# Kernel tuning notes

Hardware: AMD Instinct MI355X
Metric: run time of the kernel (lower is better)

## Reference

```python
import jax, jax.numpy as jnp
import numpy as np

N_HEAD = 16
LN_EPS = 1e-5


def _layernorm(x, g, b):
    mu = jnp.mean(x, axis=-1, keepdims=True)
    var = jnp.mean(jnp.square(x - mu), axis=-1, keepdims=True)
    return (x - mu) * jax.lax.rsqrt(var + LN_EPS) * g + b


def setup_inputs() -> dict:
    key = jax.random.key(0)
    ks = jax.random.split(key, 8)
    B, T, C = 2, 2048, 1024
    Dff = 4 * C
    s = 0.02
    return {
        "x": jax.random.normal(ks[0], (B, T, C), jnp.float32),
        "wq": jax.random.normal(ks[1], (C, C), jnp.float32) * s,
        "wk": jax.random.normal(ks[2], (C, C), jnp.float32) * s,
        "wv": jax.random.normal(ks[3], (C, C), jnp.float32) * s,
        "w_proj": jax.random.normal(ks[4], (C, C), jnp.float32) * s,
        "b_proj": jnp.zeros((C,), jnp.float32),
        "w1": jax.random.normal(ks[5], (C, Dff), jnp.float32) * s,
        "b1": jnp.zeros((Dff,), jnp.float32),
        "w2": jax.random.normal(ks[6], (Dff, C), jnp.float32) * s,
        "b2": jnp.zeros((C,), jnp.float32),
        "g1": jnp.ones((C,), jnp.float32),
        "be1": jnp.zeros((C,), jnp.float32),
        "g2": jnp.ones((C,), jnp.float32),
        "be2": jnp.zeros((C,), jnp.float32),
    }


def reference(x, wq, wk, wv, w_proj, b_proj, w1, b1, w2, b2, g1, be1, g2, be2):
    B, T, C = x.shape
    H = N_HEAD
    hd = C // H
    # QKV projections (all heads folded into one matmul each), -> [B,H,T,hd]
    q = (x @ wq).reshape(B, T, H, hd).transpose(0, 2, 1, 3)
    k = (x @ wk).reshape(B, T, H, hd).transpose(0, 2, 1, 3)
    v = (x @ wv).reshape(B, T, H, hd).transpose(0, 2, 1, 3)
    # scaled causal attention; scale = head_size ** -0.5 as in torch source
    scores = jnp.einsum("bhqd,bhkd->bhqk", q, k) * (hd ** -0.5)
    causal = jnp.tril(jnp.ones((T, T), bool))
    scores = jnp.where(causal, scores, jnp.finfo(scores.dtype).min)
    wei = jax.nn.softmax(scores, axis=-1)
    attn = jnp.einsum("bhqk,bhkd->bhqd", wei, v)  # [B,H,T,hd]
    attn = attn.transpose(0, 2, 1, 3).reshape(B, T, C)
    y = attn @ w_proj + b_proj
    # post-LN residuals as in Block.forward
    x = _layernorm(x + y, g1, be1)
    y = jnp.maximum(x @ w1 + b1, 0.0) @ w2 + b2
    x = _layernorm(x + y, g2, be2)
    return x
```

## Files before the change

### kernel.cpp

```cpp
#include <hip/hip_runtime.h>
#include <hip/hip_bf16.h>


typedef __attribute__((ext_vector_type(8))) short bf16x8;
typedef __attribute__((ext_vector_type(4))) float f32x4;
typedef __attribute__((ext_vector_type(4))) short short4v;

__device__ inline short f2bf(float f) {
    __hip_bfloat16 h = __float2bfloat16(f);
    return *reinterpret_cast<short*>(&h);
}


__global__ __launch_bounds__(256) void convert_f2b(const float* __restrict__ in,
                                                   short* __restrict__ out, int n4) {
    int i = blockIdx.x * 256 + threadIdx.x;
    if (i < n4) {
        float4 v = *(const float4*)(in + (size_t)i * 4);
        short4v o = { f2bf(v.x), f2bf(v.y), f2bf(v.z), f2bf(v.w) };
        *(short4v*)(out + (size_t)i * 4) = o;
    }
}

__global__ __launch_bounds__(256) void transpose4_f2b(const float* __restrict__ s0,
                                                      const float* __restrict__ s1,
                                                      const float* __restrict__ s2,
                                                      const float* __restrict__ s3,
                                                      short* __restrict__ d0,
                                                      short* __restrict__ d1,
                                                      short* __restrict__ d2,
                                                      short* __restrict__ d3,
                                                      float scale0) {
    __shared__ short tile[32][33];
    const int z = blockIdx.z;
    const float* in = z == 0 ? s0 : z == 1 ? s1 : z == 2 ? s2 : s3;
    short* out = z == 0 ? d0 : z == 1 ? d1 : z == 2 ? d2 : d3;
    const float scale = z == 0 ? scale0 : 1.0f;
    int c0 = blockIdx.x * 32, r0 = blockIdx.y * 32;
    int tx = threadIdx.x, ty = threadIdx.y;
    for (int i = ty; i < 32; i += 8)
        tile[i][tx] = f2bf(in[(size_t)(r0 + i) * 1024 + c0 + tx] * scale);
    __syncthreads();
    for (int i = ty; i < 32; i += 8)
        out[(size_t)(c0 + i) * 1024 + r0 + tx] = tile[tx][i];
}

__global__ __launch_bounds__(256) void transpose_f2b(const float* __restrict__ in,
                                                     short* __restrict__ out, int R, int C,
                                                     float scale) {
    __shared__ short tile[32][33];
    int c0 = blockIdx.x * 32, r0 = blockIdx.y * 32;
    int tx = threadIdx.x, ty = threadIdx.y;
    for (int i = ty; i < 32; i += 8)
        tile[i][tx] = f2bf(in[(size_t)(r0 + i) * C + c0 + tx] * scale);
    __syncthreads();
    for (int i = ty; i < 32; i += 8)
        out[(size_t)(c0 + i) * R + r0 + tx] = tile[tx][i];
}

__global__ __launch_bounds__(256) void transpose_b2b(const short* __restrict__ in,
                                                     short* __restrict__ out, int R, int C,
                                                     int istride) {
    __shared__ short tile[32][33];
    int c0 = blockIdx.x * 32, r0 = blockIdx.y * 32;
    int tx = threadIdx.x, ty = threadIdx.y;
    for (int i = ty; i < 32; i += 8)
        tile[i][tx] = in[(size_t)(r0 + i) * istride + c0 + tx];
    __syncthreads();
    for (int i = ty; i < 32; i += 8)
        out[(size_t)(c0 + i) * R + r0 + tx] = tile[tx][i];
}

template <int BN, int BIAS, int RELU, int OUTBF>
__global__ __launch_bounds__(256) void gemm_bt(const short* __restrict__ A,
                                               const short* __restrict__ BT,
                                               const float* __restrict__ bias,
                                               void* __restrict__ Cout,
                                               int M, int N, int K, int lda, int ldb,
                                               void* __restrict__ Cout2) {
    constexpr int NI = BN / 32;
    __shared__ short As[128 * 32];
    __shared__ short Bs[BN * 32];
    const int tid = threadIdx.x;
    const int wid = tid >> 6;
    const int lane = tid & 63;
    const int wr = wid >> 1, wc = wid & 1;
    const int kz = blockIdx.z;
    if (kz) { A += K; BT += K; Cout = Cout2; }
    const int gx = gridDim.x;
    int flat = blockIdx.x + gx * blockIdx.y;
    const int nwg = gx * gridDim.y;
    int w = flat;
    if ((nwg & 7) == 0) {
        const int q = nwg >> 3;
        w = (flat & 7) * q + (flat >> 3);
    }
    const int row0 = (w % gx) * 128;
    const int col0 = (w / gx) * BN;
    const int lr = lane & 15;
    const int lk = (lane >> 4) * 8;
    const int sr = lane >> 2;
    const int sc = (lane & 3) * 8;

    f32x4 acc[4][NI] = {};
    for (int k = 0; k < K; k += 32) {
#pragma unroll
        for (int c = 0; c < 2; ++c) {
            const int ch = wid + c * 4;
            const short* ga = A + (size_t)(row0 + ch * 16 + sr) * lda + k + sc;
            __builtin_amdgcn_global_load_lds(
                (const __attribute__((address_space(1))) unsigned int*)ga,
                (__attribute__((address_space(3))) unsigned int*)(As + ch * 512), 16, 0, 0);
        }
#pragma unroll
        for (int c = 0; c < BN / 64; ++c) {
            const int ch = wid + c * 4;
            const short* gb = BT + (size_t)(col0 + ch * 16 + sr) * ldb + k + sc;
            __builtin_amdgcn_global_load_lds(
                (const __attribute__((address_space(1))) unsigned int*)gb,
                (__attribute__((address_space(3))) unsigned int*)(Bs + ch * 512), 16, 0, 0);
        }
        __syncthreads();
        bf16x8 a[4], b[NI];
#pragma unroll
        for (int m = 0; m < 4; ++m)
            a[m] = *(const bf16x8*)(As + (wr * 64 + m * 16 + lr) * 32 + lk);
#pragma unroll
        for (int n = 0; n < NI; ++n)
            b[n] = *(const bf16x8*)(Bs + (wc * (BN / 2) + n * 16 + lr) * 32 + lk);
#pragma unroll
        for (int m = 0; m < 4; ++m)
#pragma unroll
            for (int n = 0; n < NI; ++n)
                acc[m][n] = __builtin_amdgcn_mfma_f32_16x16x32_bf16(a[m], b[n], acc[m][n], 0, 0, 0);
        __syncthreads();
    }
#pragma unroll
    for (int m = 0; m < 4; ++m) {
        int row = row0 + wr * 64 + m * 16 + (lane >> 4) * 4;
#pragma unroll
        for (int n = 0; n < NI; ++n) {
            int col = col0 + wc * (BN / 2) + n * 16 + lr;
            float bv = (BIAS && kz == 0) ? bias[col] : 0.0f;
#pragma unroll
            for (int r = 0; r < 4; ++r) {
                float v = acc[m][n][r] + bv;
                if (RELU) v = fmaxf(v, 0.0f);
                if (OUTBF)
                    ((short*)Cout)[(size_t)(row + r) * N + col] = f2bf(v);
                else
                    ((float*)Cout)[(size_t)(row + r) * N + col] = v;
            }
        }
    }
}

#define ATT_T 2048
#define ATT_QKS 3072
#define ATT_BT 4096

#define LOADK(KF, KB)                                                                     \
    do {                                                                                  \
        const int k0_ = (KB) * 64;                                                        \
        _Pragma("unroll") for (int t = 0; t < 4; ++t) {                                   \
            const size_t krow_ = (size_t)(b * ATT_T + k0_ + 16 * t + lr) * ATT_QKS + h * 64; \
            KF[t][0] = *(const bf16x8*)(Km + krow_ + g * 8);                              \
            KF[t][1] = *(const bf16x8*)(Km + krow_ + 32 + g * 8);                         \
        }                                                                                 \
    } while (0)

#define LOADV(VF, KB)                                                                     \
    do {                                                                                  \
        const int k0_ = (KB) * 64;                                                        \
        _Pragma("unroll") for (int n = 0; n < 4; ++n)                                     \
            _Pragma("unroll") for (int ks = 0; ks < 2; ++ks)                              \
                VF[n][ks] = *(const bf16x8*)(Vt + (size_t)(h * 64 + n * 16 + lr) * ATT_BT + \
                                             b * ATT_T + k0_ + ks * 32 + g * 8);          \
    } while (0)

#define COMPUTE(KF, VF, KB)                                                               \
    do {                                                                                  \
        const int k0_ = (KB) * 64;                                                        \
        const bool edge_ = (KB) == nfull;                                                 \
        _Pragma("unroll") for (int qs = 0; qs < 2; ++qs) {                                \
            f32x4 st[4];                                                                  \
            __builtin_amdgcn_s_setprio(1);                                                \
            _Pragma("unroll") for (int t = 0; t < 4; ++t) {                               \
                f32x4 s = {};                                                             \
                s = __builtin_amdgcn_mfma_f32_16x16x32_bf16(KF[t][0], aq[qs][0], s, 0, 0, 0); \
                s = __builtin_amdgcn_mfma_f32_16x16x32_bf16(KF[t][1], aq[qs][1], s, 0, 0, 0); \
                st[t] = s;                                                                \
            }                                                                             \
            __builtin_amdgcn_s_setprio(0);                                                \
            float v[4][4];                                                                \
            float mx = -3e38f;                                                            \
            if (edge_) {                                                                  \
                _Pragma("unroll") for (int t = 0; t < 4; ++t)                             \
                    _Pragma("unroll") for (int r = 0; r < 4; ++r) {                       \
                        float val = st[t][r];                                             \
                        if (k0_ + 16 * t + g * 4 + r > qrow[qs]) val = -3e38f;            \
                        v[t][r] = val;                                                    \
                        mx = fmaxf(mx, val);                                              \
                    }                                                                     \
            } else {                                                                      \
                _Pragma("unroll") for (int t = 0; t < 4; ++t)                             \
                    _Pragma("unroll") for (int r = 0; r < 4; ++r) {                       \
                        v[t][r] = st[t][r];                                               \
                        mx = fmaxf(mx, st[t][r]);                                         \
                    }                                                                     \
            }                                                                             \
            mx = fmaxf(mx, __shfl_xor(mx, 16));                                           \
            mx = fmaxf(mx, __shfl_xor(mx, 32));                                           \
            if (!__all(mx <= mrun[qs] + 8.0f)) {                                          \
                const float mnew = fmaxf(mrun[qs], mx);                                   \
                const float alpha = exp2f(mrun[qs] - mnew);                               \
                mrun[qs] = mnew;                                                          \
                lrun[qs] *= alpha;                                                        \
                _Pragma("unroll") for (int n = 0; n < 4; ++n)                             \
                    _Pragma("unroll") for (int r = 0; r < 4; ++r) O[qs][n][r] *= alpha;   \
            }                                                                             \
            const float m0 = mrun[qs];                                                    \
            float rs = 0.0f;                                                              \
            _Pragma("unroll") for (int t = 0; t < 4; ++t) {                               \
                short4v pw;                                                               \
                _Pragma("unroll") for (int r = 0; r < 4; ++r) {                           \
                    float p = exp2f(v[t][r] - m0);                                        \
                    rs += p;                                                              \
                    pw[r] = f2bf(p);                                                      \
                }                                                                         \
                *(short4v*)(&Plds[wid][qs][lr][16 * t + g * 4]) = pw;                     \
            }                                                                             \
            rs += __shfl_xor(rs, 16);                                                     \
            rs += __shfl_xor(rs, 32);                                                     \
            lrun[qs] += rs;                                                               \
        }                                                                                 \
        asm volatile("s_waitcnt lgkmcnt(0)" ::: "memory");                                \
        __builtin_amdgcn_sched_barrier(0);                                                \
        __builtin_amdgcn_s_setprio(1);                                                    \
        _Pragma("unroll") for (int qs = 0; qs < 2; ++qs)                                  \
            _Pragma("unroll") for (int ks = 0; ks < 2; ++ks) {                            \
                bf16x8 pf = *(const bf16x8*)(&Plds[wid][qs][lr][ks * 32 + g * 8]);        \
                _Pragma("unroll") for (int n = 0; n < 4; ++n)                             \
                    O[qs][n] = __builtin_amdgcn_mfma_f32_16x16x32_bf16(VF[n][ks], pf, O[qs][n], 0, 0, 0); \
            }                                                                             \
        __builtin_amdgcn_s_setprio(0);                                                    \
    } while (0)

__global__ __launch_bounds__(128) void flash_attn(const short* __restrict__ Q,
                                                  const short* __restrict__ Km,
                                                  const short* __restrict__ Vt,
                                                  short* __restrict__ Oout) {
    const int f = blockIdx.x;
    const int wid = threadIdx.x >> 6;
    const int lane = threadIdx.x & 63;
    const int lr = lane & 15;
    const int g = lane >> 4;
    const int xcd = f & 7;
    const int k = f >> 3;
    const int bh = xcd * 4 + (k & 3);
    const int b = bh >> 4;
    const int h = bh & 15;
    const int pair = (k >> 2) * 2 + wid;

    __shared__ __align__(16) short Plds[2][2][16][72];

#pragma unroll 1
    for (int job = 0; job < 2; ++job) {
        const int s = job ? (63 - pair) : pair;
        const int q0 = s << 5;
        const int qrow[2] = { q0 + lr, q0 + 16 + lr };
        const int nfull = s >> 1;

        bf16x8 aq[2][2];
#pragma unroll
        for (int qs = 0; qs < 2; ++qs)
#pragma unroll
            for (int ds = 0; ds < 2; ++ds)
                aq[qs][ds] = *(const bf16x8*)(Q + (size_t)(b * ATT_T + q0 + qs * 16 + lr) * ATT_QKS +
                                              h * 64 + ds * 32 + g * 8);

        f32x4 O[2][4] = {};
        float mrun[2] = { -1e30f, -1e30f }, lrun[2] = { 0.0f, 0.0f };

        bf16x8 kfA[4][2], kfB[4][2], vf[4][2];
        LOADK(kfA, 0);
        int kb = 0;
        while (true) {
            LOADV(vf, kb);
            if (kb < nfull) LOADK(kfB, kb + 1);
            COMPUTE(kfA, vf, kb);
            ++kb;
            if (kb > nfull) break;
            LOADV(vf, kb);
            if (kb < nfull) LOADK(kfA, kb + 1);
            COMPUTE(kfB, vf, kb);
            ++kb;
            if (kb > nfull) break;
        }

#pragma unroll
        for (int qs = 0; qs < 2; ++qs) {
            const float inv = 1.0f / lrun[qs];
#pragma unroll
            for (int n = 0; n < 4; ++n) {
                short4v ov;
#pragma unroll
                for (int r = 0; r < 4; ++r) ov[r] = f2bf(O[qs][n][r] * inv);
                *(short4v*)(Oout + (size_t)(b * ATT_T + q0 + qs * 16 + lr) * 1024 +
                            h * 64 + n * 16 + g * 4) = ov;
            }
        }
    }
}

__global__ __launch_bounds__(256) void resid_ln(const float* __restrict__ x,
                                                const float* __restrict__ y,
                                                const float* __restrict__ yb,
                                                const float* __restrict__ g,
                                                const float* __restrict__ be,
                                                float* __restrict__ of,
                                                short* __restrict__ ob) {
    const int row = blockIdx.x;
    const int tid = threadIdx.x;
    const size_t base = (size_t)row * 1024 + tid * 4;
    float4 xv = *(const float4*)(x + base);
    float4 yv = *(const float4*)(y + base);
    float h0 = xv.x + yv.x, h1 = xv.y + yv.y, h2 = xv.z + yv.z, h3 = xv.w + yv.w;
    if (yb) {
        float4 bv2 = *(const float4*)(yb + base);
        h0 += bv2.x; h1 += bv2.y; h2 += bv2.z; h3 += bv2.w;
    }
    float s = h0 + h1 + h2 + h3;
    float ss = h0 * h0 + h1 * h1 + h2 * h2 + h3 * h3;
#pragma unroll
    for (int d = 1; d < 64; d <<= 1) {
        s += __shfl_xor(s, d);
        ss += __shfl_xor(ss, d);
    }
    __shared__ float as_[4], ass_[4];
    if ((tid & 63) == 0) { as_[tid >> 6] = s; ass_[tid >> 6] = ss; }
    __syncthreads();
    s = as_[0] + as_[1] + as_[2] + as_[3];
    ss = ass_[0] + ass_[1] + ass_[2] + ass_[3];
    const float mu = s * (1.0f / 1024.0f);
    const float var = ss * (1.0f / 1024.0f) - mu * mu;
    const float rstd = rsqrtf(var + 1e-5f);
    float4 gv = *(const float4*)(g + tid * 4);
    float4 bv = *(const float4*)(be + tid * 4);
    float o0 = (h0 - mu) * rstd * gv.x + bv.x;
    float o1 = (h1 - mu) * rstd * gv.y + bv.y;
    float o2 = (h2 - mu) * rstd * gv.z + bv.z;
    float o3 = (h3 - mu) * rstd * gv.w + bv.w;
    float4 ov = { o0, o1, o2, o3 };
    *(float4*)(of + base) = ov;
    if (ob) {
        short4v obv = { f2bf(o0), f2bf(o1), f2bf(o2), f2bf(o3) };
        *(short4v*)(ob + base) = obv;
    }
}


extern "C" void kernel_launch(void* const* d_in, const int* in_sizes, int n_in,
                              void* d_out, int out_size, void* d_ws, size_t ws_size,
                              hipStream_t stream) {
    const float* x = (const float*)d_in[0];
    const float* wq = (const float*)d_in[1];
    const float* wk = (const float*)d_in[2];
    const float* wv = (const float*)d_in[3];
    const float* wp = (const float*)d_in[4];
    const float* bproj = (const float*)d_in[5];
    const float* w1 = (const float*)d_in[6];
    const float* b1 = (const float*)d_in[7];
    const float* w2 = (const float*)d_in[8];
    const float* b2 = (const float*)d_in[9];
    const float* g1 = (const float*)d_in[10];
    const float* be1 = (const float*)d_in[11];
    const float* g2 = (const float*)d_in[12];
    const float* be2 = (const float*)d_in[13];

    char* ws = (char*)d_ws;
    const size_t MB = 1024 * 1024;
    short* x_bf = (short*)(ws + 0);
    short* wqkvT = (short*)(ws + 8 * MB);
    short* wqT = wqkvT;
    short* wkT = (short*)(ws + 10 * MB);
    short* wvT = (short*)(ws + 12 * MB);
    short* wpT = (short*)(ws + 14 * MB);
    short* w1T = (short*)(ws + 16 * MB);
    short* w2T = (short*)(ws + 24 * MB);
    short* qkv = (short*)(ws + 32 * MB);
    short* Vt  = (short*)(ws + 56 * MB);
    short* hbf = (short*)(ws + 32 * MB);
    short* attn = (short*)(ws + 64 * MB);
    short* x1bf = (short*)(ws + 64 * MB);
    float* y1 = (float*)(ws + 72 * MB);
    float* y2a = (float*)(ws + 72 * MB);
    float* y2b = (float*)(ws + 0);
    float* x1f = (float*)(ws + 88 * MB);

    dim3 blk(256);
    dim3 tb(32, 8);
    const float SC = 0.125f * 1.44269504089f;

    convert_f2b<<<dim3(4096), blk, 0, stream>>>(x, x_bf, 4096 * 1024 / 4);
    transpose4_f2b<<<dim3(32, 32, 4), tb, 0, stream>>>(wq, wk, wv, wp, wqT, wkT, wvT, wpT, SC);
    transpose_f2b<<<dim3(128, 32), tb, 0, stream>>>(w1, w1T, 1024, 4096, 1.0f);
    transpose_f2b<<<dim3(32, 128), tb, 0, stream>>>(w2, w2T, 4096, 1024, 1.0f);

    gemm_bt<128, 0, 0, 1><<<dim3(32, 24), blk, 0, stream>>>(x_bf, wqkvT, nullptr, qkv,
                                                            4096, 3072, 1024, 1024, 1024, nullptr);
    transpose_b2b<<<dim3(32, 128), tb, 0, stream>>>(qkv + 2048, Vt, 4096, 1024, 3072);
    flash_attn<<<dim3(512), dim3(128), 0, stream>>>(qkv, qkv + 1024, Vt, attn);
    gemm_bt<64, 1, 0, 0><<<dim3(32, 16), blk, 0, stream>>>(attn, wpT, bproj, y1,
                                                           4096, 1024, 1024, 1024, 1024, nullptr);
    resid_ln<<<dim3(4096), blk, 0, stream>>>(x, y1, nullptr, g1, be1, x1f, x1bf);
    gemm_bt<128, 1, 1, 1><<<dim3(32, 32), blk, 0, stream>>>(x1bf, w1T, b1, hbf,
                                                            4096, 4096, 1024, 1024, 1024, nullptr);
    gemm_bt<64, 1, 0, 0><<<dim3(32, 16, 2), blk, 0, stream>>>(hbf, w2T, b2, y2a,
                                                              4096, 1024, 2048, 4096, 4096, y2b);
    resid_ln<<<dim3(4096), blk, 0, stream>>>(x1f, y2a, y2b, g2, be2, (float*)d_out, nullptr);
}
```

Baseline: 300.8 us.

## Compute V transposed directly in QKV GEMM, widen GEMM K tile with LDS swizzle

Replaces the separate QKV GEMM plus V transpose with one fused launch. Some blocks compute Q/K, and the others compute Vt directly as wvT·x^T, which removes the transpose kernel and its extra memory traffic. The shared GEMM core now stages 64-wide K tiles using an XOR swizzle, which halves the number of barriers per K and aims to reduce LDS bank conflicts. The attention-projection GEMM gets a split-K of 2, adding more blocks at the cost of an extra fp32 partial buffer summed in the layernorm.

```diff
diff --git a/kernel.cpp b/kernel.cpp
--- a/kernel.cpp
+++ b/kernel.cpp
@@ -58,17 +58,82 @@
         out[(size_t)(c0 + i) * R + r0 + tx] = tile[tx][i];
 }
 
-__global__ __launch_bounds__(256) void transpose_b2b(const short* __restrict__ in,
-                                                     short* __restrict__ out, int R, int C,
-                                                     int istride) {
-    __shared__ short tile[32][33];
-    int c0 = blockIdx.x * 32, r0 = blockIdx.y * 32;
-    int tx = threadIdx.x, ty = threadIdx.y;
-    for (int i = ty; i < 32; i += 8)
-        tile[i][tx] = in[(size_t)(r0 + i) * istride + c0 + tx];
-    __syncthreads();
-    for (int i = ty; i < 32; i += 8)
-        out[(size_t)(c0 + i) * R + r0 + tx] = tile[tx][i];
+template <int BN, int BIAS, int RELU, int OUTBF>
+__device__ __forceinline__ void gemm_core(const short* __restrict__ A,
+                                          const short* __restrict__ BT,
+                                          const float* __restrict__ bias,
+                                          void* __restrict__ Cout,
+                                          int N, int K, int lda, int ldb,
+                                          int gx, int w,
+                                          short* As, short* Bs, bool addbias) {
+    constexpr int NI = BN / 32;
+    const int tid = threadIdx.x;
+    const int wid = tid >> 6;
+    const int lane = tid & 63;
+    const int wr = wid >> 1, wc = wid & 1;
+    const int row0 = (w % gx) * 128;
+    const int col0 = (w / gx) * BN;
+    const int lr = lane & 15;
+    const int lk = (lane >> 4) * 8;
+    const int sr = lane >> 3;
+    const int scs = ((lane & 7) * 8) ^ (sr * 8);
+    const int rsw = (lr & 7) * 8;
+
+    f32x4 acc[4][NI] = {};
+    for (int k = 0; k < K; k += 64) {
+#pragma unroll
+        for (int c = 0; c < 4; ++c) {
+            const int ch = wid + c * 4;
+            const short* ga = A + (size_t)(row0 + ch * 8 + sr) * lda + k + scs;
+            __builtin_amdgcn_global_load_lds(
+                (const __attribute__((address_space(1))) unsigned int*)ga,
+                (__attribute__((address_space(3))) unsigned int*)(As + ch * 512), 16, 0, 0);
+        }
+#pragma unroll
+        for (int c = 0; c < BN / 32; ++c) {
+            const int ch = wid + c * 4;
+            const short* gb = BT + (size_t)(col0 + ch * 8 + sr) * ldb + k + scs;
+            __builtin_amdgcn_global_load_lds(
+                (const __attribute__((address_space(1))) unsigned int*)gb,
+                (__attribute__((address_space(3))) unsigned int*)(Bs + ch * 512), 16, 0, 0);
+        }
+        __syncthreads();
+#pragma unroll
+        for (int kk = 0; kk < 64; kk += 32) {
+            const int cof = (kk + lk) ^ rsw;
+            bf16x8 a[4], b[NI];
+#pragma unroll
+            for (int m = 0; m < 4; ++m)
+                a[m] = *(const bf16x8*)(As + (wr * 64 + m * 16 + lr) * 64 + cof);
+#pragma unroll
+            for (int n = 0; n < NI; ++n)
+                b[n] = *(const bf16x8*)(Bs + (wc * (BN / 2) + n * 16 + lr) * 64 + cof);
+#pragma unroll
+            for (int m = 0; m < 4; ++m)
+#pragma unroll
+                for (int n = 0; n < NI; ++n)
+                    acc[m][n] = __builtin_amdgcn_mfma_f32_16x16x32_bf16(a[m], b[n], acc[m][n], 0, 0, 0);
+        }
+        __syncthreads();
+    }
+#pragma unroll
+    for (int m = 0; m < 4; ++m) {
+        int row = row0 + wr * 64 + m * 16 + (lane >> 4) * 4;
+#pragma unroll
+        for (int n = 0; n < NI; ++n) {
+            int col = col0 + wc * (BN / 2) + n * 16 + lr;
+            float bv = (BIAS && addbias) ? bias[col] : 0.0f;
+#pragma unroll
+            for (int r = 0; r < 4; ++r) {
+                float v = acc[m][n][r] + bv;
+                if (RELU) v = fmaxf(v, 0.0f);
+                if (OUTBF)
+                    ((short*)Cout)[(size_t)(row + r) * N + col] = f2bf(v);
+                else
+                    ((float*)Cout)[(size_t)(row + r) * N + col] = v;
+            }
+        }
+    }
 }
 
 template <int BN, int BIAS, int RELU, int OUTBF>
@@ -76,15 +141,10 @@
                                                const short* __restrict__ BT,
                                                const float* __restrict__ bias,
                                                void* __restrict__ Cout,
-                                               int M, int N, int K, int lda, int ldb,
+                                               int N, int K, int lda, int ldb,
                                                void* __restrict__ Cout2) {
-    constexpr int NI = BN / 32;
-    __shared__ short As[128 * 32];
-    __shared__ short Bs[BN * 32];
-    const int tid = threadIdx.x;
-    const int wid = tid >> 6;
-    const int lane = tid & 63;
-    const int wr = wid >> 1, wc = wid & 1;
+    __shared__ short As[128 * 64];
+    __shared__ short Bs[BN * 64];
     const int kz = blockIdx.z;
     if (kz) { A += K; BT += K; Cout = Cout2; }
     const int gx = gridDim.x;
@@ -95,68 +155,29 @@
         const int q = nwg >> 3;
         w = (flat & 7) * q + (flat >> 3);
     }
-    const int row0 = (w % gx) * 128;
-    const int col0 = (w / gx) * BN;
-    const int lr = lane & 15;
-    const int lk = (lane >> 4) * 8;
-    const int sr = lane >> 2;
-    const int sc = (lane & 3) * 8;
-
-    f32x4 acc[4][NI] = {};
-    for (int k = 0; k < K; k += 32) {
-#pragma unroll
-        for (int c = 0; c < 2; ++c) {
-            const int ch = wid + c * 4;
-            const short* ga = A + (size_t)(row0 + ch * 16 + sr) * lda + k + sc;
-            __builtin_amdgcn_global_load_lds(
-                (const __attribute__((address_space(1))) unsigned int*)ga,
-                (__attribute__((address_space(3))) unsigned int*)(As + ch * 512), 16, 0, 0);
-        }
-#pragma unroll
-        for (int c = 0; c < BN / 64; ++c) {
-            const int ch = wid + c * 4;
-            const short* gb = BT + (size_t)(col0 + ch * 16 + sr) * ldb + k + sc;
-            __builtin_amdgcn_global_load_lds(
-                (const __attribute__((address_space(1))) unsigned int*)gb,
-                (__attribute__((address_space(3))) unsigned int*)(Bs + ch * 512), 16, 0, 0);
-        }
-        __syncthreads();
-        bf16x8 a[4], b[NI];
-#pragma unroll
-        for (int m = 0; m < 4; ++m)
-            a[m] = *(const bf16x8*)(As + (wr * 64 + m * 16 + lr) * 32 + lk);
-#pragma unroll
-        for (int n = 0; n < NI; ++n)
-            b[n] = *(const bf16x8*)(Bs + (wc * (BN / 2) + n * 16 + lr) * 32 + lk);
-#pragma unroll
-        for (int m = 0; m < 4; ++m)
-#pragma unroll
-            for (int n = 0; n < NI; ++n)
-                acc[m][n] = __builtin_amdgcn_mfma_f32_16x16x32_bf16(a[m], b[n], acc[m][n], 0, 0, 0);
-        __syncthreads();
-    }
-#pragma unroll
-    for (int m = 0; m < 4; ++m) {
-        int row = row0 + wr * 64 + m * 16 + (lane >> 4) * 4;
-#pragma unroll
-        for (int n = 0; n < NI; ++n) {
-            int col = col0 + wc * (BN / 2) + n * 16 + lr;
-            float bv = (BIAS && kz == 0) ? bias[col] : 0.0f;
-#pragma unroll
-            for (int r = 0; r < 4; ++r) {
-                float v = acc[m][n][r] + bv;
-                if (RELU) v = fmaxf(v, 0.0f);
-                if (OUTBF)
-                    ((short*)Cout)[(size_t)(row + r) * N + col] = f2bf(v);
-                else
-                    ((float*)Cout)[(size_t)(row + r) * N + col] = v;
-            }
-        }
+    gemm_core<BN, BIAS, RELU, OUTBF>(A, BT, bias, Cout, N, K, lda, ldb, gx, w, As, Bs, kz == 0);
+}
+
+__global__ __launch_bounds__(256) void gemm_qkv_vt(const short* __restrict__ x_bf,
+                                                   const short* __restrict__ wqkT,
+                                                   const short* __restrict__ wvT,
+                                                   short* __restrict__ qk,
+                                                   short* __restrict__ Vt) {
+    __shared__ short As[128 * 64];
+    __shared__ short Bs[128 * 64];
+    int flat = blockIdx.x;
+    if (flat < 512) {
+        const int w = (flat & 7) * 64 + (flat >> 3);
+        gemm_core<128, 0, 0, 1>(x_bf, wqkT, nullptr, qk, 2048, 1024, 1024, 1024, 32, w, As, Bs, false);
+    } else {
+        flat -= 512;
+        const int w = (flat & 7) * 32 + (flat >> 3);
+        gemm_core<128, 0, 0, 1>(wvT, x_bf, nullptr, Vt, 4096, 1024, 1024, 1024, 8, w, As, Bs, false);
     }
 }
 
 #define ATT_T 2048
-#define ATT_QKS 3072
+#define ATT_QKS 2048
 #define ATT_BT 4096
 
 #define LOADK(KF, KB)                                                                     \
@@ -381,19 +402,20 @@
     char* ws = (char*)d_ws;
     const size_t MB = 1024 * 1024;
     short* x_bf = (short*)(ws + 0);
-    short* wqkvT = (short*)(ws + 8 * MB);
-    short* wqT = wqkvT;
+    short* wqkT = (short*)(ws + 8 * MB);
+    short* wqT = wqkT;
     short* wkT = (short*)(ws + 10 * MB);
     short* wvT = (short*)(ws + 12 * MB);
-    short* wpT = (short*)(ws + 14 * MB);
     short* w1T = (short*)(ws + 16 * MB);
     short* w2T = (short*)(ws + 24 * MB);
-    short* qkv = (short*)(ws + 32 * MB);
+    short* qk  = (short*)(ws + 32 * MB);
+    short* wpT = (short*)(ws + 48 * MB);
     short* Vt  = (short*)(ws + 56 * MB);
     short* hbf = (short*)(ws + 32 * MB);
     short* attn = (short*)(ws + 64 * MB);
     short* x1bf = (short*)(ws + 64 * MB);
-    float* y1 = (float*)(ws + 72 * MB);
+    float* y1a = (float*)(ws + 72 * MB);
+    float* y1b = (float*)(ws + 0);
     float* y2a = (float*)(ws + 72 * MB);
     float* y2b = (float*)(ws + 0);
     float* x1f = (float*)(ws + 88 * MB);
@@ -407,16 +429,14 @@
     transpose_f2b<<<dim3(128, 32), tb, 0, stream>>>(w1, w1T, 1024, 4096, 1.0f);
     transpose_f2b<<<dim3(32, 128), tb, 0, stream>>>(w2, w2T, 4096, 1024, 1.0f);
 
-    gemm_bt<128, 0, 0, 1><<<dim3(32, 24), blk, 0, stream>>>(x_bf, wqkvT, nullptr, qkv,
-                                                            4096, 3072, 1024, 1024, 1024, nullptr);
-    transpose_b2b<<<dim3(32, 128), tb, 0, stream>>>(qkv + 2048, Vt, 4096, 1024, 3072);
-    flash_attn<<<dim3(512), dim3(128), 0, stream>>>(qkv, qkv + 1024, Vt, attn);
-    gemm_bt<64, 1, 0, 0><<<dim3(32, 16), blk, 0, stream>>>(attn, wpT, bproj, y1,
-                                                           4096, 1024, 1024, 1024, 1024, nullptr);
-    resid_ln<<<dim3(4096), blk, 0, stream>>>(x, y1, nullptr, g1, be1, x1f, x1bf);
+    gemm_qkv_vt<<<dim3(768), blk, 0, stream>>>(x_bf, wqkT, wvT, qk, Vt);
+    flash_attn<<<dim3(512), dim3(128), 0, stream>>>(qk, qk + 1024, Vt, attn);
+    gemm_bt<64, 1, 0, 0><<<dim3(32, 16, 2), blk, 0, stream>>>(attn, wpT, bproj, y1a,
+                                                              1024, 512, 1024, 1024, y1b);
+    resid_ln<<<dim3(4096), blk, 0, stream>>>(x, y1a, y1b, g1, be1, x1f, x1bf);
     gemm_bt<128, 1, 1, 1><<<dim3(32, 32), blk, 0, stream>>>(x1bf, w1T, b1, hbf,
-                                                            4096, 4096, 1024, 1024, 1024, nullptr);
+                                                            4096, 1024, 1024, 1024, nullptr);
     gemm_bt<64, 1, 0, 0><<<dim3(32, 16, 2), blk, 0, stream>>>(hbf, w2T, b2, y2a,
-                                                              4096, 1024, 2048, 4096, 4096, y2b);
+                                                              1024, 2048, 4096, 4096, y2b);
     resid_ln<<<dim3(4096), blk, 0, stream>>>(x1f, y2a, y2b, g2, be2, (float*)d_out, nullptr);
 }
```

New measurement: 295.1 us. Within noise of the previous version (-1.9%).
